# Kernel tuning notes

Hardware: AMD Instinct MI355X
Metric: run time of the kernel (lower is better)

Reference implementation:

```python
import jax, jax.numpy as jnp
import numpy as np

D = 2048
H = 16
HD = D // H
FF = 4 * D
EPS = 1e-5


def layernorm(x, scale, shift):
    mean = jnp.mean(x, axis=-1, keepdims=True)
    var = jnp.mean((x - mean) ** 2, axis=-1, keepdims=True)  # unbiased=False
    return scale * (x - mean) / jnp.sqrt(var + EPS) + shift


def setup_inputs() -> dict:
    key = jax.random.key(0)
    ks = jax.random.split(key, 12)
    s = 0.02
    return {
        "x": jax.random.normal(ks[0], (2, 2048, D), dtype=jnp.float32),
        "ln1_scale": jnp.ones((D,), jnp.float32),
        "ln1_shift": jnp.zeros((D,), jnp.float32),
        "wq": jax.random.normal(ks[1], (D, D), jnp.float32) * s,
        "bq": jnp.zeros((D,), jnp.float32),
        "wk": jax.random.normal(ks[2], (D, D), jnp.float32) * s,
        "bk": jnp.zeros((D,), jnp.float32),
        "wv": jax.random.normal(ks[3], (D, D), jnp.float32) * s,
        "bv": jnp.zeros((D,), jnp.float32),
        "wo": jax.random.normal(ks[4], (D, D), jnp.float32) * s,
        "bo": jnp.zeros((D,), jnp.float32),
        "ln2_scale": jnp.ones((D,), jnp.float32),
        "ln2_shift": jnp.zeros((D,), jnp.float32),
        "w1": jax.random.normal(ks[5], (D, FF), jnp.float32) * s,
        "b1": jnp.zeros((FF,), jnp.float32),
        "w2": jax.random.normal(ks[6], (FF, D), jnp.float32) * s,
        "b2": jnp.zeros((D,), jnp.float32),
    }


def block(x, ln1_scale, ln1_shift, wq, bq, wk, bk, wv, bv, wo, bo,
          ln2_scale, ln2_shift, w1, b1, w2, b2):
    B, S, _ = x.shape
    h = layernorm(x, ln1_scale, ln1_shift)
    q = (h @ wq + bq).reshape(B, S, H, HD).transpose(0, 2, 1, 3)  # [B,H,S,hd]
    k = (h @ wk + bk).reshape(B, S, H, HD).transpose(0, 2, 1, 3)
    v = (h @ wv + bv).reshape(B, S, H, HD).transpose(0, 2, 1, 3)
    scores = jnp.einsum("bhqd,bhkd->bhqk", q, k) / jnp.sqrt(jnp.float32(HD))
    causal = jnp.tril(jnp.ones((S, S), dtype=bool))
    scores = jnp.where(causal[None, None], scores, -jnp.inf)
    attn = jax.nn.softmax(scores, axis=-1)
    ctx = jnp.einsum("bhqk,bhkd->bhqd", attn, v)
    ctx = ctx.transpose(0, 2, 1, 3).reshape(B, S, D)
    x = x + (ctx @ wo + bo)
    h2 = layernorm(x, ln2_scale, ln2_shift)
    ffn = jax.nn.gelu(h2 @ w1 + b1, approximate=False) @ w2 + b2
    return x + ffn


def reference(x, ln1_scale, ln1_shift, wq, bq, wk, bk, wv, bv, wo, bo,
              ln2_scale, ln2_shift, w1, b1, w2, b2):
    return block(x, ln1_scale, ln1_shift, wq, bq, wk, bk, wv, bv, wo, bo,
                 ln2_scale, ln2_shift, w1, b1, w2, b2)
```

## Files before the change

### kernel.cpp

```cpp
#include <hip/hip_runtime.h>
#include <hip/hip_bf16.h>
#include <math.h>

namespace {

constexpr int Dm  = 2048;
constexpr int FFm = 8192;
constexpr int SEQ = 2048;
constexpr int HDm = 128;
constexpr int MR  = 4096;
constexpr int QW  = 3 * Dm;

typedef __bf16 bf16_t;
typedef __bf16 bf16x8 __attribute__((ext_vector_type(8)));
typedef float  f32x4  __attribute__((ext_vector_type(4)));

typedef __attribute__((address_space(1))) const void as1_void;
typedef __attribute__((address_space(3))) void as3_void;

__device__ __forceinline__ void gload_lds16(const void* g, void* l) {
  __builtin_amdgcn_global_load_lds((as1_void*)g, (as3_void*)l, 16, 0, 0);
}

__global__ __launch_bounds__(256)
void ln_kernel(const float* __restrict__ x, const float* __restrict__ sc,
               const float* __restrict__ sh, bf16_t* __restrict__ out)
{
  const int row = blockIdx.x;
  const int tid = threadIdx.x;
  const float4* xr = (const float4*)(x + (size_t)row * Dm);
  float4 v0 = xr[tid*2], v1 = xr[tid*2+1];
  float s  = v0.x+v0.y+v0.z+v0.w + v1.x+v1.y+v1.z+v1.w;
  float s2 = v0.x*v0.x+v0.y*v0.y+v0.z*v0.z+v0.w*v0.w
           + v1.x*v1.x+v1.y*v1.y+v1.z*v1.z+v1.w*v1.w;
  #pragma unroll
  for (int off = 32; off; off >>= 1) { s += __shfl_xor(s, off); s2 += __shfl_xor(s2, off); }
  __shared__ float red[8];
  if ((tid & 63) == 0) { red[(tid>>6)*2] = s; red[(tid>>6)*2+1] = s2; }
  __syncthreads();
  s  = red[0]+red[2]+red[4]+red[6];
  s2 = red[1]+red[3]+red[5]+red[7];
  const float mean = s * (1.f/Dm);
  const float var  = fmaxf(s2 * (1.f/Dm) - mean*mean, 0.f);
  const float rstd = rsqrtf(var + 1e-5f);
  const float4* scp = (const float4*)sc;
  const float4* shp = (const float4*)sh;
  float4 sc0 = scp[tid*2], sc1 = scp[tid*2+1];
  float4 sh0 = shp[tid*2], sh1 = shp[tid*2+1];
  __attribute__((aligned(16))) bf16_t ob[8];
  ob[0] = (bf16_t)((v0.x-mean)*rstd*sc0.x + sh0.x);
  ob[1] = (bf16_t)((v0.y-mean)*rstd*sc0.y + sh0.y);
  ob[2] = (bf16_t)((v0.z-mean)*rstd*sc0.z + sh0.z);
  ob[3] = (bf16_t)((v0.w-mean)*rstd*sc0.w + sh0.w);
  ob[4] = (bf16_t)((v1.x-mean)*rstd*sc1.x + sh1.x);
  ob[5] = (bf16_t)((v1.y-mean)*rstd*sc1.y + sh1.y);
  ob[6] = (bf16_t)((v1.z-mean)*rstd*sc1.z + sh1.z);
  ob[7] = (bf16_t)((v1.w-mean)*rstd*sc1.w + sh1.w);
  *(uint4*)(out + (size_t)row*Dm + tid*8) = *(const uint4*)ob;
}

__global__ __launch_bounds__(256)
void ln_fused(const float* __restrict__ p0, const float* __restrict__ p1,
              const float* __restrict__ bias, const float* __restrict__ resid,
              const float* __restrict__ sc, const float* __restrict__ sh,
              float* __restrict__ x1, bf16_t* __restrict__ out)
{
  const int row = blockIdx.x;
  const int tid = threadIdx.x;
  const size_t base = (size_t)row * Dm + tid*8;
  float v[8];
  #pragma unroll
  for (int hh = 0; hh < 2; ++hh) {
    float4 a  = *(const float4*)(p0 + base + hh*4);
    float4 b  = *(const float4*)(p1 + base + hh*4);
    float4 r  = *(const float4*)(resid + base + hh*4);
    float4 bv = *(const float4*)(bias + tid*8 + hh*4);
    v[hh*4+0] = a.x + b.x + bv.x + r.x;
    v[hh*4+1] = a.y + b.y + bv.y + r.y;
    v[hh*4+2] = a.z + b.z + bv.z + r.z;
    v[hh*4+3] = a.w + b.w + bv.w + r.w;
  }
  *(float4*)(x1 + base)     = *(const float4*)&v[0];
  *(float4*)(x1 + base + 4) = *(const float4*)&v[4];
  float s = 0.f, s2 = 0.f;
  #pragma unroll
  for (int j = 0; j < 8; ++j) { s += v[j]; s2 += v[j]*v[j]; }
  #pragma unroll
  for (int off = 32; off; off >>= 1) { s += __shfl_xor(s, off); s2 += __shfl_xor(s2, off); }
  __shared__ float red[8];
  if ((tid & 63) == 0) { red[(tid>>6)*2] = s; red[(tid>>6)*2+1] = s2; }
  __syncthreads();
  s  = red[0]+red[2]+red[4]+red[6];
  s2 = red[1]+red[3]+red[5]+red[7];
  const float mean = s * (1.f/Dm);
  const float var  = fmaxf(s2 * (1.f/Dm) - mean*mean, 0.f);
  const float rstd = rsqrtf(var + 1e-5f);
  __attribute__((aligned(16))) bf16_t ob[8];
  #pragma unroll
  for (int hh = 0; hh < 2; ++hh) {
    float4 scv = *(const float4*)(sc + tid*8 + hh*4);
    float4 shv = *(const float4*)(sh + tid*8 + hh*4);
    ob[hh*4+0] = (bf16_t)((v[hh*4+0]-mean)*rstd*scv.x + shv.x);
    ob[hh*4+1] = (bf16_t)((v[hh*4+1]-mean)*rstd*scv.y + shv.y);
    ob[hh*4+2] = (bf16_t)((v[hh*4+2]-mean)*rstd*scv.z + shv.z);
    ob[hh*4+3] = (bf16_t)((v[hh*4+3]-mean)*rstd*scv.w + shv.w);
  }
  *(uint4*)(out + base) = *(const uint4*)ob;
}

__global__ __launch_bounds__(256)
void wconv4(const float* __restrict__ wq, const float* __restrict__ wk,
            const float* __restrict__ wv, const float* __restrict__ wo,
            bf16_t* __restrict__ dst)
{
  const int z = blockIdx.z;
  const float* W = (z == 0) ? wq : (z == 1) ? wk : (z == 2) ? wv : wo;
  bf16_t* WT = dst + (size_t)z * Dm * Dm;
  __shared__ float tile[32][33];
  const int tx = threadIdx.x & 31, ty = threadIdx.x >> 5;
  const int nb = blockIdx.x * 32, kb = blockIdx.y * 32;
  #pragma unroll
  for (int p = 0; p < 4; ++p)
    tile[ty+8*p][tx] = W[(size_t)(kb+ty+8*p)*Dm + nb + tx];
  __syncthreads();
  #pragma unroll
  for (int p = 0; p < 4; ++p)
    WT[(size_t)(nb+ty+8*p)*Dm + kb + tx] = (bf16_t)tile[tx][ty+8*p];
}

__global__ __launch_bounds__(256)
void wconv_t(const float* __restrict__ W, bf16_t* __restrict__ WT, int K, int N)
{
  __shared__ float tile[32][33];
  const int tx = threadIdx.x & 31, ty = threadIdx.x >> 5;
  const int nb = blockIdx.x * 32, kb = blockIdx.y * 32;
  #pragma unroll
  for (int p = 0; p < 4; ++p)
    tile[ty+8*p][tx] = W[(size_t)(kb+ty+8*p)*N + nb + tx];
  __syncthreads();
  #pragma unroll
  for (int p = 0; p < 4; ++p)
    WT[(size_t)(nb+ty+8*p)*K + kb + tx] = (bf16_t)tile[tx][ty+8*p];
}

__global__ void bias_concat(const float* __restrict__ bq, const float* __restrict__ bk,
                            const float* __restrict__ bv, float* __restrict__ o)
{
  int i = blockIdx.x*256 + threadIdx.x;
  o[i] = bq[i]; o[Dm+i] = bk[i]; o[2*Dm+i] = bv[i];
}

__global__ __launch_bounds__(256)
void vtrans(const bf16_t* __restrict__ qkv, bf16_t* __restrict__ vT)
{
  __shared__ bf16_t tile[32][33];
  const int tx = threadIdx.x & 31, ty = threadIdx.x >> 5;
  const int s0 = blockIdx.x*32, d0 = blockIdx.y*32, bh = blockIdx.z;
  const int b = bh >> 4, h = bh & 15;
  const bf16_t* src = qkv + (size_t)(b*SEQ)*QW + 2*Dm + h*HDm;
  #pragma unroll
  for (int p = 0; p < 4; ++p)
    tile[ty+8*p][tx] = src[(size_t)(s0+ty+8*p)*QW + d0 + tx];
  __syncthreads();
  bf16_t* dst = vT + (size_t)bh*HDm*SEQ;
  #pragma unroll
  for (int p = 0; p < 4; ++p)
    dst[(size_t)(d0+ty+8*p)*SEQ + s0 + tx] = tile[tx][ty+8*p];
}

template<int MODE>
__global__ __launch_bounds__(512, 2)
void gemm8p(const bf16_t* __restrict__ A, const bf16_t* __restrict__ BT,
            const float* __restrict__ bias,
            void* __restrict__ Cout, void* __restrict__ Cout2,
            int Ndim, int Kslice, int Kstride, int gn)
{
  const int gm = (int)gridDim.x / gn;
  const int cm = gm >> 1, cn = gn >> 2;
  const int c = blockIdx.x & 7;
  const int idx = blockIdx.x >> 3;
  const int mi = idx / cn, ni = idx - mi*cn;
  const int m0 = ((c >> 2)*cm + mi) * 256;
  const int n0 = ((c & 3)*cn + ni) * 256;
  const int kOff = blockIdx.y * Kslice;
  const int tid = threadIdx.x;
  const int lane = tid & 63;
  const int w = tid >> 6;
  const int wr = w >> 2, wc = w & 3;
  const int lr = lane & 15, kg = lane >> 4;

  __shared__ __attribute__((aligned(16))) bf16_t lds[65536];

  f32x4 acc[8][4] = {};

  const int r1   = tid >> 3;
  const int blk1 = (tid & 7) ^ (r1 & 7);
  const size_t rowoff = (size_t)64 * Kstride;
  const bf16_t* pA0 = A  + (size_t)(m0 + r1)*Kstride       + kOff + blk1*8;
  const bf16_t* pA1 = A  + (size_t)(m0 + 128 + r1)*Kstride + kOff + blk1*8;
  const bf16_t* pB0 = BT + (size_t)(n0 + r1)*Kstride       + kOff + blk1*8;
  const bf16_t* pB1 = BT + (size_t)(n0 + 128 + r1)*Kstride + kOff + blk1*8;
  bf16_t* const d0 = lds + (size_t)tid*8;

#define STG(p, region) do { \
    gload_lds16((p), d0 + (size_t)(region)*8192); \
    gload_lds16((p) + rowoff, d0 + (size_t)(region)*8192 + 4096); \
    (p) += 64; } while (0)

  auto readA = [&](int buf, int mh, bf16x8* f) {
    #pragma unroll
    for (int ml = 0; ml < 4; ++ml)
      #pragma unroll
      for (int kk = 0; kk < 2; ++kk) {
        const bf16_t* base = lds + (buf*4 + mh)*8192;
        const int row = wr*64 + ml*16 + lr;
        f[ml*2+kk] = *(const bf16x8*)(base + row*64 + (((kk*4+kg) ^ (row&7))*8));
      }
  };
  auto readB = [&](int buf, int nh, bf16x8* f) {
    #pragma unroll
    for (int nl = 0; nl < 2; ++nl)
      #pragma unroll
      for (int kk = 0; kk < 2; ++kk) {
        const bf16_t* base = lds + (buf*4 + 2 + nh)*8192;
        const int row = wc*32 + nl*16 + lr;
        f[nl*2+kk] = *(const bf16x8*)(base + row*64 + (((kk*4+kg) ^ (row&7))*8));
      }
  };
  auto mfma16 = [&](int mh, int nh, const bf16x8* Af, const bf16x8* Bf) {
    __builtin_amdgcn_s_setprio(1);
    #pragma unroll
    for (int ml = 0; ml < 4; ++ml)
      #pragma unroll
      for (int nl = 0; nl < 2; ++nl)
        #pragma unroll
        for (int kk = 0; kk < 2; ++kk)
          acc[mh*4+ml][nh*2+nl] =
            __builtin_amdgcn_mfma_f32_16x16x32_bf16(Af[ml*2+kk], Bf[nl*2+kk],
                                                    acc[mh*4+ml][nh*2+nl], 0, 0, 0);
    __builtin_amdgcn_s_setprio(0);
  };

#define BAR() __builtin_amdgcn_s_barrier()
#define LGKM0() asm volatile("s_waitcnt lgkmcnt(0)")

  bf16x8 Af0[8], Af1[8], Bf0[4], Bf1[4];
  bf16x8 Af0b[8], Af1b[8], Bf0b[4], Bf1b[4];

  STG(pA0, 0); STG(pA1, 1); STG(pB0, 2); STG(pB1, 3);
  STG(pA0, 4); STG(pA1, 5); STG(pB0, 6); STG(pB1, 7);
  asm volatile("s_waitcnt vmcnt(8)" ::: "memory");
  BAR();

  const int NITER = Kslice >> 7;
  for (int j = 0; j < NITER; ++j) {
    const bool s2 = (j + 1 < NITER);

    readA(0, 0, Af0); readB(0, 0, Bf0);
    BAR(); LGKM0(); mfma16(0, 0, Af0, Bf0); BAR();

    readB(0, 1, Bf1);
    if (s2) STG(pA0, 0);
    BAR(); LGKM0(); mfma16(0, 1, Af0, Bf1); BAR();

    readA(0, 1, Af1);
    if (s2) STG(pB0, 2);
    BAR(); LGKM0(); mfma16(1, 1, Af1, Bf1);
    if (s2) asm volatile("s_waitcnt vmcnt(4)" ::: "memory");
    else    asm volatile("s_waitcnt vmcnt(0)" ::: "memory");
    BAR();

    readA(1, 0, Af0b);
    if (s2) { STG(pA1, 1); STG(pB1, 3); }
    BAR(); LGKM0(); mfma16(1, 0, Af1, Bf0); BAR();

    readB(1, 0, Bf0b);
    BAR(); LGKM0(); mfma16(0, 0, Af0b, Bf0b); BAR();

    readB(1, 1, Bf1b);
    if (s2) { STG(pA0, 4); STG(pB0, 6); }
    BAR(); LGKM0(); mfma16(0, 1, Af0b, Bf1b); BAR();

    readA(1, 1, Af1b);
    if (s2) STG(pB1, 7);
    BAR(); LGKM0(); mfma16(1, 1, Af1b, Bf1b); BAR();

    if (s2) STG(pA1, 5);
    BAR(); mfma16(1, 0, Af1b, Bf0b);
    if (s2) asm volatile("s_waitcnt vmcnt(8)" ::: "memory");
    else    asm volatile("s_waitcnt vmcnt(0)" ::: "memory");
    BAR();
  }
#undef STG
#undef BAR
#undef LGKM0

  if constexpr (MODE == 0 || MODE == 1) {
    __syncthreads();
    #pragma unroll
    for (int NF = 0; NF < 4; ++NF) {
      const int col = (NF>>1)*128 + wc*32 + (NF&1)*16 + lr;
      const float bv = bias[n0 + col];
      #pragma unroll
      for (int MF = 0; MF < 8; ++MF) {
        #pragma unroll
        for (int jj = 0; jj < 4; ++jj) {
          float v = acc[MF][NF][jj] + bv;
          if constexpr (MODE == 1) v = 0.5f*v*(1.f + erff(v*0.70710678118f));
          const int row = (MF>>2)*128 + wr*64 + (MF&3)*16 + kg*4 + jj;
          const int adr = row*256 + (((col >> 3) ^ (row & 7)) << 3) + (col & 7);
          lds[adr] = (bf16_t)v;
        }
      }
    }
    __syncthreads();
    bf16_t* outp = (bf16_t*)Cout;
    #pragma unroll
    for (int i = 0; i < 16; ++i) {
      const int s = tid + i*512;
      const int row = s >> 5, ch = s & 31;
      uint4 vv = *(const uint4*)(lds + row*256 + ((ch ^ (row & 7)) << 3));
      *(uint4*)(outp + (size_t)(m0 + row)*Ndim + n0 + ch*8) = vv;
    }
  } else {
    float* pout = (float*)(blockIdx.y ? Cout2 : Cout);
    #pragma unroll
    for (int NF = 0; NF < 4; ++NF) {
      const int col = n0 + (NF>>1)*128 + wc*32 + (NF&1)*16 + lr;
      #pragma unroll
      for (int MF = 0; MF < 8; ++MF) {
        const int rbase = m0 + (MF>>2)*128 + wr*64 + (MF&3)*16 + kg*4;
        #pragma unroll
        for (int jj = 0; jj < 4; ++jj)
          pout[(size_t)(rbase + jj)*Ndim + col] = acc[MF][NF][jj];
      }
    }
  }
}

__global__ __launch_bounds__(256)
void splitk_reduce(const float* __restrict__ p0, const float* __restrict__ p1,
                   const float* __restrict__ bias, const float* __restrict__ resid,
                   float* __restrict__ out, int Ndim)
{
  const size_t e = ((size_t)blockIdx.x*256 + threadIdx.x) * 4;
  float4 a = *(const float4*)(p0 + e);
  float4 b = *(const float4*)(p1 + e);
  float4 r = *(const float4*)(resid + e);
  float4 bv = *(const float4*)(bias + (int)(e & (size_t)(Ndim - 1)));
  float4 o;
  o.x = a.x + b.x + bv.x + r.x;
  o.y = a.y + b.y + bv.y + r.y;
  o.z = a.z + b.z + bv.z + r.z;
  o.w = a.w + b.w + bv.w + r.w;
  *(float4*)(out + e) = o;
}

__global__ __launch_bounds__(512)
void flash_attn7(const bf16_t* __restrict__ qkv, const bf16_t* __restrict__ vT,
                 bf16_t* __restrict__ ctx)
{
  const int bid = blockIdx.x;
  const int bh  = (bid & 7) + 8 * ((bid >> 3) & 3);
  const int pr  = bid >> 5;
  const int b = bh >> 4, h = bh & 15;
  const int tid = threadIdx.x;
  const int lane = tid & 63;
  const int w = tid >> 6;
  const int wg = w >> 2;
  const int wsub = w & 3;
  const int lr = lane & 15, kg = lane >> 4;

  const int qi = wg ? (15 - pr) : pr;
  const int Q0 = qi * 128;
  const int q0w = Q0 + wsub * 32;

  __shared__ __attribute__((aligned(16))) bf16_t Ks[2][64*128];
  __shared__ __attribute__((aligned(16))) bf16_t Vs[2][128*64];
  __shared__ __attribute__((aligned(16))) bf16_t Plds[8*2048];

  const bf16_t* kbase = qkv + (size_t)(b*SEQ)*QW + Dm + h*HDm;
  const bf16_t* vbase = vT + (size_t)bh*HDm*SEQ;
  const float scl = 0.08838834764831845f * 1.44269504089f;

  auto stage = [&](int buf, int k0) {
    #pragma unroll
    for (int i = 0; i < 2; ++i) {
      const int s = tid + i*512;
      const int row = s >> 4, sl = s & 15;
      gload_lds16(kbase + (size_t)(k0 + row)*QW + (sl ^ (row & 7))*8, Ks[buf] + s*8);
    }
    #pragma unroll
    for (int i = 0; i < 2; ++i) {
      const int s = tid + i*512;
      const int row = s >> 3, sl = s & 7;
      gload_lds16(vbase + (size_t)row*SEQ + k0 + (sl ^ (row & 7))*8, Vs[buf] + s*8);
    }
  };

  bf16x8 qf[2][4];
  #pragma unroll
  for (int rt = 0; rt < 2; ++rt) {
    const bf16_t* qb = qkv + (size_t)(b*SEQ + q0w + rt*16 + lr)*QW + h*HDm;
    #pragma unroll
    for (int g = 0; g < 4; ++g)
      qf[rt][g] = *(const bf16x8*)(qb + g*32 + kg*8);
  }

  float mrow[2][4], lsum[2][4];
  f32x4 oacc[2][8];
  #pragma unroll
  for (int rt = 0; rt < 2; ++rt) {
    #pragma unroll
    for (int j = 0; j < 4; ++j) { mrow[rt][j] = -INFINITY; lsum[rt][j] = 0.f; }
    #pragma unroll
    for (int dt = 0; dt < 8; ++dt) oacc[rt][dt] = (f32x4){0.f,0.f,0.f,0.f};
  }

  const int NT = (16 - pr) * 2;
  stage(0, 0);
  asm volatile("s_waitcnt vmcnt(0)" ::: "memory");
  __syncthreads();
  for (int t = 0; t < NT; ++t) {
    const int k0 = t * 64;
    const int buf = t & 1;
    const bool more = (t + 1 < NT);
    if (more) stage(buf ^ 1, k0 + 64);
    if (k0 < q0w + 32) {
      f32x4 sa[2][4];
      #pragma unroll
      for (int rt = 0; rt < 2; ++rt)
        #pragma unroll
        for (int ct = 0; ct < 4; ++ct) sa[rt][ct] = (f32x4){0.f,0.f,0.f,0.f};
      #pragma unroll
      for (int ct = 0; ct < 4; ++ct) {
        const int krow = ct*16 + lr;
        #pragma unroll
        for (int g = 0; g < 4; ++g) {
          bf16x8 kf = *(const bf16x8*)(Ks[buf] + krow*128 + ((4*g + kg) ^ (krow & 7))*8);
          sa[0][ct] = __builtin_amdgcn_mfma_f32_16x16x32_bf16(qf[0][g], kf, sa[0][ct], 0, 0, 0);
          sa[1][ct] = __builtin_amdgcn_mfma_f32_16x16x32_bf16(qf[1][g], kf, sa[1][ct], 0, 0, 0);
        }
      }
      #pragma unroll
      for (int rt = 0; rt < 2; ++rt)
        #pragma unroll
        for (int ct = 0; ct < 4; ++ct)
          #pragma unroll
          for (int j = 0; j < 4; ++j) sa[rt][ct][j] *= scl;
      if (k0 + 63 > q0w) {
        #pragma unroll
        for (int ct = 0; ct < 4; ++ct) {
          const int kidx = k0 + ct*16 + lr;
          #pragma unroll
          for (int rt = 0; rt < 2; ++rt)
            #pragma unroll
            for (int j = 0; j < 4; ++j) {
              const int qidx = q0w + rt*16 + kg*4 + j;
              if (kidx > qidx) sa[rt][ct][j] = -INFINITY;
            }
        }
      }
      #pragma unroll
      for (int rt = 0; rt < 2; ++rt) {
        #pragma unroll
        for (int j = 0; j < 4; ++j) {
          const int prow = kg*4 + j;
          float x0 = sa[rt][0][j], x1 = sa[rt][1][j], x2 = sa[rt][2][j], x3 = sa[rt][3][j];
          float v = fmaxf(fmaxf(x0, x1), fmaxf(x2, x3));
          v = fmaxf(v, __shfl_xor(v, 1));
          v = fmaxf(v, __shfl_xor(v, 2));
          v = fmaxf(v, __shfl_xor(v, 4));
          v = fmaxf(v, __shfl_xor(v, 8));
          const float mn = fmaxf(mrow[rt][j], v);
          const float alpha = exp2f(mrow[rt][j] - mn);
          mrow[rt][j] = mn;
          float p0 = exp2f(x0 - mn), p1 = exp2f(x1 - mn);
          float p2 = exp2f(x2 - mn), p3 = exp2f(x3 - mn);
          float ss = (p0 + p1) + (p2 + p3);
          ss += __shfl_xor(ss, 1);
          ss += __shfl_xor(ss, 2);
          ss += __shfl_xor(ss, 4);
          ss += __shfl_xor(ss, 8);
          lsum[rt][j] = lsum[rt][j]*alpha + ss;
          #pragma unroll
          for (int dt = 0; dt < 8; ++dt) oacc[rt][dt][j] *= alpha;
          const int base = w*2048 + rt*1024 + prow*64;
          const int sw = (prow & 7) << 3;
          Plds[(base + ( 0 + lr)) ^ sw] = (bf16_t)p0;
          Plds[(base + (16 + lr)) ^ sw] = (bf16_t)p1;
          Plds[(base + (32 + lr)) ^ sw] = (bf16_t)p2;
          Plds[(base + (48 + lr)) ^ sw] = (bf16_t)p3;
        }
      }
      bf16x8 pf[2][2];
      {
        const int sw = (lr & 7) << 3;
        #pragma unroll
        for (int rt = 0; rt < 2; ++rt) {
          pf[rt][0] = *(const bf16x8*)(Plds + ((w*2048 + rt*1024 + lr*64 +      kg*8) ^ sw));
          pf[rt][1] = *(const bf16x8*)(Plds + ((w*2048 + rt*1024 + lr*64 + 32 + kg*8) ^ sw));
        }
      }
      #pragma unroll
      for (int dt = 0; dt < 8; ++dt) {
        const int vrow = dt*16 + lr;
        #pragma unroll
        for (int kc = 0; kc < 2; ++kc) {
          bf16x8 vf = *(const bf16x8*)(Vs[buf] + vrow*64 + ((4*kc + kg) ^ (vrow & 7))*8);
          oacc[0][dt] = __builtin_amdgcn_mfma_f32_16x16x32_bf16(pf[0][kc], vf, oacc[0][dt], 0, 0, 0);
          oacc[1][dt] = __builtin_amdgcn_mfma_f32_16x16x32_bf16(pf[1][kc], vf, oacc[1][dt], 0, 0, 0);
        }
      }
    }
    if (more) asm volatile("s_waitcnt vmcnt(0)" ::: "memory");
    __syncthreads();
  }

  #pragma unroll
  for (int rt = 0; rt < 2; ++rt) {
    bf16_t* cb = ctx + (size_t)(b*SEQ + q0w + rt*16 + kg*4)*Dm + h*HDm;
    #pragma unroll
    for (int j = 0; j < 4; ++j) {
      const float inv = 1.f / lsum[rt][j];
      #pragma unroll
      for (int dt = 0; dt < 8; ++dt)
        cb[(size_t)j*Dm + dt*16 + lr] = (bf16_t)(oacc[rt][dt][j] * inv);
    }
  }
}

}

extern "C" void kernel_launch(void* const* d_in, const int* in_sizes, int n_in,
                              void* d_out, int out_size, void* d_ws, size_t ws_size,
                              hipStream_t stream)
{
  const float* x   = (const float*)d_in[0];
  const float* g1  = (const float*)d_in[1];
  const float* s1  = (const float*)d_in[2];
  const float* wq  = (const float*)d_in[3];
  const float* bq  = (const float*)d_in[4];
  const float* wk  = (const float*)d_in[5];
  const float* bk  = (const float*)d_in[6];
  const float* wv  = (const float*)d_in[7];
  const float* bv  = (const float*)d_in[8];
  const float* wo  = (const float*)d_in[9];
  const float* bo  = (const float*)d_in[10];
  const float* g2  = (const float*)d_in[11];
  const float* s2  = (const float*)d_in[12];
  const float* w1  = (const float*)d_in[13];
  const float* b1  = (const float*)d_in[14];
  const float* w2  = (const float*)d_in[15];
  const float* b2  = (const float*)d_in[16];
  float* out = (float*)d_out;

  char* p = (char*)d_ws;
  bf16_t* wqkvT = (bf16_t*)p;  p += (size_t)QW*Dm*2;
  bf16_t* woT   = (bf16_t*)p;  p += (size_t)Dm*Dm*2;
  bf16_t* w1T   = (bf16_t*)p;  p += (size_t)FFm*Dm*2;
  bf16_t* w2T   = (bf16_t*)p;  p += (size_t)Dm*FFm*2;
  float*  bqkv  = (float*)p;   p += (size_t)QW*4;
  bf16_t* hbuf  = (bf16_t*)p;  p += (size_t)MR*Dm*2;
  bf16_t* qkv   = (bf16_t*)p;  p += (size_t)MR*QW*2;
  bf16_t* vTb   = (bf16_t*)p;  p += (size_t)32*HDm*SEQ*2;
  bf16_t* ctx   = (bf16_t*)p;  p += (size_t)MR*Dm*2;
  float*  x1    = (float*)p;   p += (size_t)MR*Dm*4;
  bf16_t* ffn1  = qkv;
  float*  prj0  = (float*)qkv;
  float*  prj1  = (float*)qkv + (size_t)MR*Dm;
  float*  f2p0  = (float*)w1T;
  float*  f2p1  = (float*)wqkvT;

  wconv4<<<dim3(Dm/32, Dm/32, 4), 256, 0, stream>>>(wq, wk, wv, wo, wqkvT);
  wconv_t<<<dim3(FFm/32, Dm/32), 256, 0, stream>>>(w1, w1T, Dm, FFm);
  wconv_t<<<dim3(Dm/32, FFm/32), 256, 0, stream>>>(w2, w2T, FFm, Dm);
  bias_concat<<<dim3(Dm/256), 256, 0, stream>>>(bq, bk, bv, bqkv);

  ln_kernel<<<dim3(MR), 256, 0, stream>>>(x, g1, s1, hbuf);
  gemm8p<0><<<dim3((QW/256)*(MR/256), 1), 512, 0, stream>>>(
      hbuf, wqkvT, bqkv, qkv, nullptr, QW, Dm, Dm, QW/256);
  vtrans<<<dim3(SEQ/32, HDm/32, 32), 256, 0, stream>>>(qkv, vTb);
  flash_attn7<<<dim3(256), 512, 0, stream>>>(qkv, vTb, ctx);
  gemm8p<3><<<dim3((Dm/256)*(MR/256), 2), 512, 0, stream>>>(
      ctx, woT, nullptr, prj0, prj1, Dm, Dm/2, Dm, Dm/256);
  ln_fused<<<dim3(MR), 256, 0, stream>>>(prj0, prj1, bo, x, g2, s2, x1, hbuf);
  gemm8p<1><<<dim3((FFm/256)*(MR/256), 1), 512, 0, stream>>>(
      hbuf, w1T, b1, ffn1, nullptr, FFm, Dm, Dm, FFm/256);
  gemm8p<3><<<dim3((Dm/256)*(MR/256), 2), 512, 0, stream>>>(
      ffn1, w2T, nullptr, f2p0, f2p1, Dm, FFm/2, FFm, Dm/256);
  splitk_reduce<<<dim3(MR*Dm/1024), 256, 0, stream>>>(f2p0, f2p1, b2, x1, out, Dm);
}
```

Baseline: 659.6 us.

## Split QKV GEMM into QK GEMM plus split-K V GEMM with fused transpose

New measurement: 646.8 us. No clear change (-1.9%).

```diff
diff --git a/kernel.cpp b/kernel.cpp
--- a/kernel.cpp
+++ b/kernel.cpp
@@ -151,16 +151,20 @@
 }
 
 __global__ __launch_bounds__(256)
-void vtrans(const bf16_t* __restrict__ qkv, bf16_t* __restrict__ vT)
+void vtrans_fused(const bf16_t* __restrict__ vp0, const bf16_t* __restrict__ vp1,
+                  const float* __restrict__ bv, bf16_t* __restrict__ vT)
 {
   __shared__ bf16_t tile[32][33];
   const int tx = threadIdx.x & 31, ty = threadIdx.x >> 5;
   const int s0 = blockIdx.x*32, d0 = blockIdx.y*32, bh = blockIdx.z;
   const int b = bh >> 4, h = bh & 15;
-  const bf16_t* src = qkv + (size_t)(b*SEQ)*QW + 2*Dm + h*HDm;
-  #pragma unroll
-  for (int p = 0; p < 4; ++p)
-    tile[ty+8*p][tx] = src[(size_t)(s0+ty+8*p)*QW + d0 + tx];
+  const int gd = h*HDm + d0 + tx;
+  const float bias = bv[gd];
+  #pragma unroll
+  for (int p = 0; p < 4; ++p) {
+    const size_t idx = (size_t)(b*SEQ + s0 + ty + 8*p)*Dm + gd;
+    tile[ty+8*p][tx] = (bf16_t)((float)vp0[idx] + (float)vp1[idx] + bias);
+  }
   __syncthreads();
   bf16_t* dst = vT + (size_t)bh*HDm*SEQ;
   #pragma unroll
@@ -295,12 +299,13 @@
 #undef BAR
 #undef LGKM0
 
-  if constexpr (MODE == 0 || MODE == 1) {
+  if constexpr (MODE == 0 || MODE == 1 || MODE == 4) {
     __syncthreads();
     #pragma unroll
     for (int NF = 0; NF < 4; ++NF) {
       const int col = (NF>>1)*128 + wc*32 + (NF&1)*16 + lr;
-      const float bv = bias[n0 + col];
+      float bv = 0.f;
+      if constexpr (MODE != 4) bv = bias[n0 + col];
       #pragma unroll
       for (int MF = 0; MF < 8; ++MF) {
         #pragma unroll
@@ -314,7 +319,9 @@
       }
     }
     __syncthreads();
-    bf16_t* outp = (bf16_t*)Cout;
+    bf16_t* outp;
+    if constexpr (MODE == 4) outp = (bf16_t*)(blockIdx.y ? Cout2 : Cout);
+    else                     outp = (bf16_t*)Cout;
     #pragma unroll
     for (int i = 0; i < 16; ++i) {
       const int s = tid + i*512;
@@ -571,6 +578,8 @@
   float*  prj1  = (float*)qkv + (size_t)MR*Dm;
   float*  f2p0  = (float*)w1T;
   float*  f2p1  = (float*)wqkvT;
+  bf16_t* vp0   = (bf16_t*)x1;
+  bf16_t* vp1   = (bf16_t*)x1 + (size_t)MR*Dm;
 
   wconv4<<<dim3(Dm/32, Dm/32, 4), 256, 0, stream>>>(wq, wk, wv, wo, wqkvT);
   wconv_t<<<dim3(FFm/32, Dm/32), 256, 0, stream>>>(w1, w1T, Dm, FFm);
@@ -578,9 +587,11 @@
   bias_concat<<<dim3(Dm/256), 256, 0, stream>>>(bq, bk, bv, bqkv);
 
   ln_kernel<<<dim3(MR), 256, 0, stream>>>(x, g1, s1, hbuf);
-  gemm8p<0><<<dim3((QW/256)*(MR/256), 1), 512, 0, stream>>>(
-      hbuf, wqkvT, bqkv, qkv, nullptr, QW, Dm, Dm, QW/256);
-  vtrans<<<dim3(SEQ/32, HDm/32, 32), 256, 0, stream>>>(qkv, vTb);
+  gemm8p<0><<<dim3((4096/256)*(MR/256), 1), 512, 0, stream>>>(
+      hbuf, wqkvT, bqkv, qkv, nullptr, QW, Dm, Dm, 4096/256);
+  gemm8p<4><<<dim3((Dm/256)*(MR/256), 2), 512, 0, stream>>>(
+      hbuf, wqkvT + (size_t)2*Dm*Dm, nullptr, vp0, vp1, Dm, Dm/2, Dm, Dm/256);
+  vtrans_fused<<<dim3(SEQ/32, HDm/32, 32), 256, 0, stream>>>(vp0, vp1, bv, vTb);
   flash_attn7<<<dim3(256), 512, 0, stream>>>(qkv, vTb, ctx);
   gemm8p<3><<<dim3((Dm/256)*(MR/256), 2), 512, 0, stream>>>(
       ctx, woT, nullptr, prj0, prj1, Dm, Dm/2, Dm, Dm/256);
```
